# Performance work log

Measured on AMD Instinct MI355X. Metric: run time of the kernel, lower is better.

The kernel has to match this reference:

```python
import jax, jax.numpy as jnp
import numpy as np

NHEAD = 16

def setup_inputs() -> dict:
    key = jax.random.key(0)
    ks = jax.random.split(key, 7)
    b, l, d = 4, 2048, 1024
    s = 1.0 / np.sqrt(d)
    return {
        "Q": jax.random.normal(ks[0], (b, l, d), jnp.float32),
        "K": jax.random.normal(ks[1], (b, l, d), jnp.float32),
        "V": jax.random.normal(ks[2], (b, l, d), jnp.float32),
        "WQ": jax.random.normal(ks[3], (d, d), jnp.float32) * s,
        "WK": jax.random.normal(ks[4], (d, d), jnp.float32) * s,
        "WV": jax.random.normal(ks[5], (d, d), jnp.float32) * s,
        "WO": jax.random.normal(ks[6], (d, d), jnp.float32) * s,
    }

def reference(Q, K, V, WQ, WK, WV, WO):
    # WQ/WK/WV/WO stored torch-style as [out, in]; Linear(x) = x @ W.T
    b, lq, d = Q.shape
    lk = K.shape[1]
    h = NHEAD
    dk = d // h
    # project and split heads: [b, l, h, dk]
    q = (Q @ WQ.T).reshape(b, lq, h, dk)
    k = (K @ WK.T).reshape(b, lk, h, dk)
    v = (V @ WV.T).reshape(b, lk, h, dk)
    # scaled dot-product attention (dropout = identity in eval mode)
    scale = 1.0 / jnp.sqrt(jnp.asarray(dk, Q.dtype))
    score = jnp.einsum('bqhd,bkhd->bhqk', q, k) * scale  # [b,h,lq,lk]
    attn = jax.nn.softmax(score, axis=-1)
    o = jnp.einsum('bhqk,bkhd->bqhd', attn, v).reshape(b, lq, h * dk)
    return o @ WO.T
```

## Files before the change

### kernel.cpp

```cpp
#include <hip/hip_runtime.h>
#include <stdint.h>

#define D_MODEL 1024
#define NHEADS 16
#define DKH 64
#define SEQ 2048
#define BATCH 4
#define M_TOT (BATCH * SEQ)
#define LOG2E 1.44269504088896340736f

typedef __bf16 v8bf __attribute__((ext_vector_type(8)));
typedef __bf16 v4bf __attribute__((ext_vector_type(4)));
typedef _Float16 v8h __attribute__((ext_vector_type(8)));
typedef _Float16 v4h __attribute__((ext_vector_type(4)));
typedef float v4f __attribute__((ext_vector_type(4)));
typedef float v16f __attribute__((ext_vector_type(16)));
typedef unsigned int v4u __attribute__((ext_vector_type(4)));
typedef unsigned int v2u __attribute__((ext_vector_type(2)));

typedef const __attribute__((address_space(1))) void* gas_ptr;
typedef __attribute__((address_space(3))) void* las_ptr;

static __device__ __forceinline__ void async16(const void* g, void* l) {
    __builtin_amdgcn_global_load_lds((gas_ptr)g, (las_ptr)l, 16, 0, 0);
}

static __device__ __forceinline__ v4f mfma16x32(v8bf a, v8bf b, v4f c) {
    return __builtin_amdgcn_mfma_f32_16x16x32_bf16(a, b, c, 0, 0, 0);
}
static __device__ __forceinline__ v16f mfma32x16bf(v8bf a, v8bf b, v16f c) {
    return __builtin_amdgcn_mfma_f32_32x32x16_bf16(a, b, c, 0, 0, 0);
}
static __device__ __forceinline__ v16f mfma32x16h(v8h a, v8h b, v16f c) {
    return __builtin_amdgcn_mfma_f32_32x32x16_f16(a, b, c, 0, 0, 0);
}
static __device__ __forceinline__ unsigned pkh(float a, float b) {
    return __builtin_bit_cast(unsigned, __builtin_amdgcn_cvt_pkrtz(a, b));
}
static __device__ __forceinline__ void plswap(unsigned& x, unsigned& y) {
    v2u r = __builtin_amdgcn_permlane32_swap(x, y, false, false);
    x = r[0];
    y = r[1];
}
static __device__ __forceinline__ float fexp2(float x) {
#if __has_builtin(__builtin_amdgcn_exp2f)
    return __builtin_amdgcn_exp2f(x);
#else
    float r;
    asm("v_exp_f32 %0, %1" : "=v"(r) : "v"(x));
    return r;
#endif
}

__global__ __launch_bounds__(256) void cvt_x(const float* __restrict__ src,
                                             __bf16* __restrict__ dst) {
    int i = blockIdx.x * 256 + threadIdx.x;
    const float4* s = (const float4*)src;
    float4 a = s[2 * i], b = s[2 * i + 1];
    v8bf o;
    o[0] = (__bf16)a.x; o[1] = (__bf16)a.y; o[2] = (__bf16)a.z; o[3] = (__bf16)a.w;
    o[4] = (__bf16)b.x; o[5] = (__bf16)b.y; o[6] = (__bf16)b.z; o[7] = (__bf16)b.w;
    *(v8bf*)(dst + (size_t)i * 8) = o;
}

__global__ __launch_bounds__(256) void cvt_w(const float* __restrict__ w0,
                                             const float* __restrict__ w1,
                                             const float* __restrict__ w2,
                                             const float* __restrict__ w3,
                                             __bf16* __restrict__ dst) {
    int gid = blockIdx.x * 256 + threadIdx.x;
    int tsel = gid >> 17;
    int off = gid & 131071;
    const float* s = (tsel == 0) ? w0 : (tsel == 1) ? w1 : (tsel == 2) ? w2 : w3;
    const float4* sp = (const float4*)s + 2 * (size_t)off;
    float4 a = sp[0], b = sp[1];
    v8bf o;
    o[0] = (__bf16)a.x; o[1] = (__bf16)a.y; o[2] = (__bf16)a.z; o[3] = (__bf16)a.w;
    o[4] = (__bf16)b.x; o[5] = (__bf16)b.y; o[6] = (__bf16)b.z; o[7] = (__bf16)b.w;
    *(v8bf*)(dst + ((size_t)tsel << 20) + (size_t)off * 8) = o;
}

__global__ __launch_bounds__(256) void cvt_all(const float* __restrict__ Q,
                                               const float* __restrict__ K,
                                               const float* __restrict__ V,
                                               const float* __restrict__ w0,
                                               const float* __restrict__ w1,
                                               const float* __restrict__ w2,
                                               const float* __restrict__ w3,
                                               __bf16* __restrict__ xq,
                                               __bf16* __restrict__ xk,
                                               __bf16* __restrict__ xv,
                                               __bf16* __restrict__ wb) {
    const int blk = blockIdx.x;
    const float* src;
    __bf16* dst;
    size_t off8;
    if (blk < 2048) {
        int gid = blk * 256 + threadIdx.x;
        int tsel = gid >> 17;
        src = (tsel == 0) ? w0 : (tsel == 1) ? w1 : (tsel == 2) ? w2 : w3;
        dst = wb + ((size_t)tsel << 20);
        off8 = (size_t)(gid & 131071);
    } else {
        int gb = blk - 2048;
        int t = gb >> 12;
        src = (t == 0) ? Q : (t == 1) ? K : V;
        dst = (t == 0) ? xq : (t == 1) ? xk : xv;
        off8 = (size_t)((gb & 4095) * 256 + threadIdx.x);
    }
    const float4* sp = (const float4*)src + 2 * off8;
    float4 a = sp[0], b = sp[1];
    v8bf o;
    o[0] = (__bf16)a.x; o[1] = (__bf16)a.y; o[2] = (__bf16)a.z; o[3] = (__bf16)a.w;
    o[4] = (__bf16)b.x; o[5] = (__bf16)b.y; o[6] = (__bf16)b.z; o[7] = (__bf16)b.w;
    *(v8bf*)(dst + off8 * 8) = o;
}

#define GEMM_KLOOP(Abase, Wbase)                                                   \
    auto stage = [&](int bi, int k0) {                                             \
        _Pragma("unroll") for (int p = 0; p < 2; ++p) {                            \
            int rb = (p * 4 + wave) * 16;                                          \
            async16(Abase + (size_t)(rb + wrow) * D_MODEL + k0, &As[bi][rb * 32]); \
            async16(Wbase + (size_t)(rb + wrow) * D_MODEL + k0, &Bs[bi][rb * 32]); \
        }                                                                          \
    };                                                                             \
    stage(0, 0);                                                                   \
    for (int it = 0; it < D_MODEL / 32; ++it) {                                    \
        const int cur = it & 1;                                                    \
        if (it + 1 < D_MODEL / 32) {                                               \
            stage(cur ^ 1, (it + 1) * 32);                                         \
            asm volatile("s_waitcnt vmcnt(4)" ::: "memory");                       \
        } else {                                                                   \
            asm volatile("s_waitcnt vmcnt(0)" ::: "memory");                       \
        }                                                                          \
        __builtin_amdgcn_s_barrier();                                              \
        __builtin_amdgcn_sched_barrier(0);                                         \
        v8bf af[4], bfr[4];                                                        \
        _Pragma("unroll") for (int mt = 0; mt < 4; ++mt)                           \
            af[mt] = *(const v8bf*)&As[cur][(mw + mt * 16 + r) * 32 + rdpos];      \
        _Pragma("unroll") for (int nt = 0; nt < 4; ++nt)                           \
            bfr[nt] = *(const v8bf*)&Bs[cur][(nw + nt * 16 + r) * 32 + rdpos];     \
        _Pragma("unroll") for (int mt = 0; mt < 4; ++mt)                           \
            _Pragma("unroll") for (int nt = 0; nt < 4; ++nt)                       \
                acc[mt][nt] = mfma16x32(af[mt], bfr[nt], acc[mt][nt]);             \
        asm volatile("s_waitcnt lgkmcnt(0)" ::: "memory");                         \
        __builtin_amdgcn_s_barrier();                                              \
    }

template <int LAYOUT>
__global__ __launch_bounds__(256) void gemm_nt(const __bf16* __restrict__ A,
                                               const __bf16* __restrict__ W,
                                               void* __restrict__ Cv, float scale) {
    const int t = threadIdx.x, lane = t & 63, wave = t >> 6;
    const int r = lane & 15, qd = lane >> 4;
    const int m0 = blockIdx.x * 128, n0 = blockIdx.y * 128;
    const int mw = (wave & 1) * 64, nw = (wave >> 1) * 64;

    __shared__ __align__(16) __bf16 As[2][128 * 32];
    __shared__ __align__(16) __bf16 Bs[2][128 * 32];

    const int wc = (lane & 3) ^ ((lane >> 3) & 3);
    const int wrow = lane >> 2;
    const int rdpos = (qd ^ ((r >> 1) & 3)) * 8;

    const __bf16* Ab = A + (size_t)m0 * D_MODEL + wc * 8;
    const __bf16* Wb = W + (size_t)n0 * D_MODEL + wc * 8;

    v4f acc[4][4] = {};
    GEMM_KLOOP(Ab, Wb)

#pragma unroll
    for (int mt = 0; mt < 4; ++mt)
#pragma unroll
        for (int nt = 0; nt < 4; ++nt) {
            int row = m0 + mw + mt * 16 + qd * 4;
            int col = n0 + nw + nt * 16 + r;
            if (LAYOUT == 0) {
                float* C = (float*)Cv;
#pragma unroll
                for (int i = 0; i < 4; ++i)
                    C[(size_t)(row + i) * D_MODEL + col] = acc[mt][nt][i];
            } else {
                int bb = row >> 11, l = row & (SEQ - 1);
                int h = col >> 6, d = col & (DKH - 1);
                if (LAYOUT == 2) {
                    _Float16* vt = (_Float16*)Cv;
                    v4h o;
#pragma unroll
                    for (int i = 0; i < 4; ++i) o[i] = (_Float16)acc[mt][nt][i];
                    *(v4h*)&vt[((size_t)((bb * NHEADS + h) * DKH + d)) * SEQ + l] = o;
                } else {
                    __bf16* dst = (__bf16*)Cv;
#pragma unroll
                    for (int i = 0; i < 4; ++i)
                        dst[(((size_t)(bb * NHEADS + h) * SEQ) + l + i) * DKH + d] =
                            (__bf16)(acc[mt][nt][i] * scale);
                }
            }
        }
}

__global__ __launch_bounds__(256) void gemm_qkv(const __bf16* __restrict__ xq,
                                                const __bf16* __restrict__ xk,
                                                const __bf16* __restrict__ xv,
                                                const __bf16* __restrict__ wb,
                                                __bf16* __restrict__ qh,
                                                __bf16* __restrict__ kh,
                                                _Float16* __restrict__ vtb, float qs) {
    const int z = blockIdx.z;
    const __bf16* A = (z == 0) ? xq : (z == 1) ? xk : xv;
    const __bf16* W = wb + (size_t)z * D_MODEL * D_MODEL;

    const int t = threadIdx.x, lane = t & 63, wave = t >> 6;
    const int r = lane & 15, qd = lane >> 4;
    const int m0 = blockIdx.x * 128, n0 = blockIdx.y * 128;
    const int mw = (wave & 1) * 64, nw = (wave >> 1) * 64;

    __shared__ __align__(16) __bf16 As[2][128 * 32];
    __shared__ __align__(16) __bf16 Bs[2][128 * 32];

    const int wc = (lane & 3) ^ ((lane >> 3) & 3);
    const int wrow = lane >> 2;
    const int rdpos = (qd ^ ((r >> 1) & 3)) * 8;

    const __bf16* Ab = A + (size_t)m0 * D_MODEL + wc * 8;
    const __bf16* Wb = W + (size_t)n0 * D_MODEL + wc * 8;

    v4f acc[4][4] = {};
    GEMM_KLOOP(Ab, Wb)

    const float scale = (z == 0) ? qs : 1.0f;
#pragma unroll
    for (int mt = 0; mt < 4; ++mt)
#pragma unroll
        for (int nt = 0; nt < 4; ++nt) {
            int row = m0 + mw + mt * 16 + qd * 4;
            int col = n0 + nw + nt * 16 + r;
            int bb = row >> 11, l = row & (SEQ - 1);
            int h = col >> 6, d = col & (DKH - 1);
            if (z == 2) {
                v4h o;
#pragma unroll
                for (int i = 0; i < 4; ++i) o[i] = (_Float16)acc[mt][nt][i];
                *(v4h*)&vtb[((size_t)((bb * NHEADS + h) * DKH + d)) * SEQ + l] = o;
            } else {
                __bf16* dst = (z == 0) ? qh : kh;
#pragma unroll
                for (int i = 0; i < 4; ++i)
                    dst[(((size_t)(bb * NHEADS + h) * SEQ) + l + i) * DKH + d] =
                        (__bf16)(acc[mt][nt][i] * scale);
            }
        }
}

__global__ __launch_bounds__(256, 2) void attn_kernel(const __bf16* __restrict__ qh,
                                                      const __bf16* __restrict__ kh,
                                                      const _Float16* __restrict__ vt,
                                                      __bf16* __restrict__ oh) {
    const int lane = threadIdx.x & 63, wave = threadIdx.x >> 6;
    const int l31 = lane & 31, hi = lane >> 5, l7 = lane & 7;
    const int id = blockIdx.x;
    const int bh = (id & 7) * 8 + ((id >> 3) & 7);
    const int q0 = (id >> 6) * 128 + wave * 32;

    __shared__ __align__(16) __bf16 Kb[2][64 * 64];
    __shared__ __align__(16) _Float16 Vb[2][64 * 64];

    const __bf16* kbh = kh + (size_t)bh * SEQ * DKH;
    const _Float16* vbh = vt + (size_t)bh * DKH * SEQ;

    v8bf qf[4];
#pragma unroll
    for (int c = 0; c < 4; ++c)
        qf[c] = *(const v8bf*)&qh[((size_t)bh * SEQ + q0 + l31) * DKH + c * 16 + hi * 8];

    v16f oacc[2] = {};
    float ps = 0.f;
    const v16f dz = {};

    const int srow = lane >> 3;
    const int sc = (lane & 7) ^ srow;

#pragma unroll
    for (int p = 0; p < 2; ++p) {
        int rb = wave * 16 + p * 8;
        async16(kbh + (size_t)(rb + srow) * DKH + sc * 8, &Kb[0][rb * 64]);
        async16(vbh + (size_t)(rb + srow) * SEQ + sc * 8, &Vb[0][rb * 64]);
    }

    for (int tt = 0; tt < SEQ / 64; ++tt) {
        const int buf = tt & 1;
        __syncthreads();
        if (tt + 1 < SEQ / 64) {
            const int t0 = (tt + 1) * 64;
#pragma unroll
            for (int p = 0; p < 2; ++p) {
                int rb = wave * 16 + p * 8;
                async16(kbh + (size_t)(t0 + rb + srow) * DKH + sc * 8, &Kb[buf ^ 1][rb * 64]);
                async16(vbh + (size_t)(rb + srow) * SEQ + t0 + sc * 8, &Vb[buf ^ 1][rb * 64]);
            }
        }
        const __bf16* Kc = Kb[buf];
        const _Float16* Vc = Vb[buf];
#pragma unroll
        for (int kb = 0; kb < 2; ++kb) {
            v8bf ka[4];
#pragma unroll
            for (int c = 0; c < 4; ++c)
                ka[c] = *(const v8bf*)&Kc[(kb * 32 + l31) * 64 + (((c * 2 + hi) ^ l7) << 3)];
            v16f d = mfma32x16bf(ka[0], qf[0], dz);
#pragma unroll
            for (int c = 1; c < 4; ++c) d = mfma32x16bf(ka[c], qf[c], d);
            float e[16];
#pragma unroll
            for (int i = 0; i < 16; ++i) e[i] = fexp2(d[i]);
            ps += (((e[0] + e[1]) + (e[2] + e[3])) + ((e[4] + e[5]) + (e[6] + e[7]))) +
                  (((e[8] + e[9]) + (e[10] + e[11])) + ((e[12] + e[13]) + (e[14] + e[15])));
            v8h pb[2];
#pragma unroll
            for (int kc = 0; kc < 2; ++kc) {
                unsigned a0 = pkh(e[kc * 8 + 0], e[kc * 8 + 1]);
                unsigned a1 = pkh(e[kc * 8 + 2], e[kc * 8 + 3]);
                unsigned b0 = pkh(e[kc * 8 + 4], e[kc * 8 + 5]);
                unsigned b1 = pkh(e[kc * 8 + 6], e[kc * 8 + 7]);
                plswap(a0, b0);
                plswap(a1, b1);
                v4u w = {a0, a1, b0, b1};
                pb[kc] = __builtin_bit_cast(v8h, w);
            }
#pragma unroll
            for (int dg = 0; dg < 2; ++dg)
#pragma unroll
                for (int kc = 0; kc < 2; ++kc) {
                    v8h va = *(const v8h*)&Vc[(dg * 32 + l31) * 64 +
                                              (((kb * 4 + kc * 2 + hi) ^ l7) << 3)];
                    oacc[dg] = mfma32x16h(va, pb[kc], oacc[dg]);
                }
        }
    }

    const int b = bh >> 4, h = bh & (NHEADS - 1);
    float tot = ps + __shfl_xor(ps, 32, 64);
    float inv = 1.0f / tot;
    int lq = q0 + l31;
    __bf16* op = oh + (((size_t)(b * SEQ + lq)) * NHEADS + h) * DKH;
#pragma unroll
    for (int dg = 0; dg < 2; ++dg)
#pragma unroll
        for (int g = 0; g < 4; ++g) {
            v4bf ov;
#pragma unroll
            for (int i = 0; i < 4; ++i) ov[i] = (__bf16)(oacc[dg][g * 4 + i] * inv);
            *(v4bf*)(op + dg * 32 + g * 8 + hi * 4) = ov;
        }
}

extern "C" void kernel_launch(void* const* d_in, const int* in_sizes, int n_in,
                              void* d_out, int out_size, void* d_ws, size_t ws_size,
                              hipStream_t stream) {
    const float* Q = (const float*)d_in[0];
    const float* K = (const float*)d_in[1];
    const float* V = (const float*)d_in[2];
    const float* WQ = (const float*)d_in[3];
    const float* WK = (const float*)d_in[4];
    const float* WV = (const float*)d_in[5];
    const float* WO = (const float*)d_in[6];
    float* out = (float*)d_out;

    const size_t elems = (size_t)M_TOT * D_MODEL;
    const size_t welems = (size_t)D_MODEL * D_MODEL;
    const size_t fused_need = 8 * welems + 6 * 2 * elems;

    dim3 gg(M_TOT / 128, D_MODEL / 128);

    if (ws_size >= fused_need) {
        __bf16* wb = (__bf16*)d_ws;
        __bf16* xq = wb + 4 * welems;
        __bf16* xk = xq + elems;
        __bf16* xv = xk + elems;
        __bf16* qh = xv + elems;
        __bf16* kh = qh + elems;
        _Float16* vtb = (_Float16*)(kh + elems);
        __bf16* oh = xq;

        cvt_all<<<14336, 256, 0, stream>>>(Q, K, V, WQ, WK, WV, WO, xq, xk, xv, wb);
        dim3 gz(M_TOT / 128, D_MODEL / 128, 3);
        gemm_qkv<<<gz, 256, 0, stream>>>(xq, xk, xv, wb, qh, kh, vtb, 0.125f * LOG2E);
        attn_kernel<<<1024, 256, 0, stream>>>(qh, kh, vtb, oh);
        gemm_nt<0><<<gg, 256, 0, stream>>>(oh, wb + 3 * welems, out, 1.0f);
    } else {
        __bf16* wb = (__bf16*)d_ws;
        __bf16* xb = wb + 4 * welems;
        __bf16* qh = xb + elems;
        __bf16* kh = qh + elems;
        _Float16* vtb = (_Float16*)(kh + elems);
        __bf16* oh = (__bf16*)(vtb + elems);

        cvt_w<<<2048, 256, 0, stream>>>(WQ, WK, WV, WO, wb);
        cvt_x<<<4096, 256, 0, stream>>>(Q, xb);
        gemm_nt<1><<<gg, 256, 0, stream>>>(xb, wb, qh, 0.125f * LOG2E);
        cvt_x<<<4096, 256, 0, stream>>>(K, xb);
        gemm_nt<1><<<gg, 256, 0, stream>>>(xb, wb + welems, kh, 1.0f);
        cvt_x<<<4096, 256, 0, stream>>>(V, xb);
        gemm_nt<2><<<gg, 256, 0, stream>>>(xb, wb + 2 * welems, vtb, 1.0f);
        attn_kernel<<<1024, 256, 0, stream>>>(qh, kh, vtb, oh);
        gemm_nt<0><<<gg, 256, 0, stream>>>(oh, wb + 3 * welems, out, 1.0f);
    }
}
```

Baseline: 344.1 us.

## Triple-buffer GEMM LDS stages and process two query tiles per attention wave

The GEMM k-loop moves from a double to a triple LDS buffer, which removes the trailing wait and barrier at the end of each iteration. The attention kernel now gives each wave 64 query rows (two 32-row tiles), so each K/V fragment loaded from LDS feeds twice as many MFMAs, and the grid is halved to 512 blocks. The cost is more registers per wave for two accumulators, lower grid parallelism, and a larger LDS footprint in the GEMMs. With three stages a buffer can be overwritten by a fast wave while a slower wave may still be reading it, since only one barrier per iteration remains.

```diff
diff --git a/kernel.cpp b/kernel.cpp
--- a/kernel.cpp
+++ b/kernel.cpp
@@ -126,9 +126,9 @@
     };                                                                             \
     stage(0, 0);                                                                   \
     for (int it = 0; it < D_MODEL / 32; ++it) {                                    \
-        const int cur = it & 1;                                                    \
+        const int cur = it % 3;                                                    \
         if (it + 1 < D_MODEL / 32) {                                               \
-            stage(cur ^ 1, (it + 1) * 32);                                         \
+            stage((it + 1) % 3, (it + 1) * 32);                                    \
             asm volatile("s_waitcnt vmcnt(4)" ::: "memory");                       \
         } else {                                                                   \
             asm volatile("s_waitcnt vmcnt(0)" ::: "memory");                       \
@@ -143,8 +143,6 @@
         _Pragma("unroll") for (int mt = 0; mt < 4; ++mt)                           \
             _Pragma("unroll") for (int nt = 0; nt < 4; ++nt)                       \
                 acc[mt][nt] = mfma16x32(af[mt], bfr[nt], acc[mt][nt]);             \
-        asm volatile("s_waitcnt lgkmcnt(0)" ::: "memory");                         \
-        __builtin_amdgcn_s_barrier();                                              \
     }
 
 template <int LAYOUT>
@@ -156,8 +154,8 @@
     const int m0 = blockIdx.x * 128, n0 = blockIdx.y * 128;
     const int mw = (wave & 1) * 64, nw = (wave >> 1) * 64;
 
-    __shared__ __align__(16) __bf16 As[2][128 * 32];
-    __shared__ __align__(16) __bf16 Bs[2][128 * 32];
+    __shared__ __align__(16) __bf16 As[3][128 * 32];
+    __shared__ __align__(16) __bf16 Bs[3][128 * 32];
 
     const int wc = (lane & 3) ^ ((lane >> 3) & 3);
     const int wrow = lane >> 2;
@@ -216,8 +214,8 @@
     const int m0 = blockIdx.x * 128, n0 = blockIdx.y * 128;
     const int mw = (wave & 1) * 64, nw = (wave >> 1) * 64;
 
-    __shared__ __align__(16) __bf16 As[2][128 * 32];
-    __shared__ __align__(16) __bf16 Bs[2][128 * 32];
+    __shared__ __align__(16) __bf16 As[3][128 * 32];
+    __shared__ __align__(16) __bf16 Bs[3][128 * 32];
 
     const int wc = (lane & 3) ^ ((lane >> 3) & 3);
     const int wrow = lane >> 2;
@@ -261,7 +259,7 @@
     const int l31 = lane & 31, hi = lane >> 5, l7 = lane & 7;
     const int id = blockIdx.x;
     const int bh = (id & 7) * 8 + ((id >> 3) & 7);
-    const int q0 = (id >> 6) * 128 + wave * 32;
+    const int q0 = (id >> 6) * 256 + wave * 64;
 
     __shared__ __align__(16) __bf16 Kb[2][64 * 64];
     __shared__ __align__(16) _Float16 Vb[2][64 * 64];
@@ -269,13 +267,16 @@
     const __bf16* kbh = kh + (size_t)bh * SEQ * DKH;
     const _Float16* vbh = vt + (size_t)bh * DKH * SEQ;
 
-    v8bf qf[4];
-#pragma unroll
-    for (int c = 0; c < 4; ++c)
-        qf[c] = *(const v8bf*)&qh[((size_t)bh * SEQ + q0 + l31) * DKH + c * 16 + hi * 8];
-
-    v16f oacc[2] = {};
-    float ps = 0.f;
+    v8bf qf[2][4];
+#pragma unroll
+    for (int qa = 0; qa < 2; ++qa)
+#pragma unroll
+        for (int c = 0; c < 4; ++c)
+            qf[qa][c] = *(const v8bf*)&qh[((size_t)bh * SEQ + q0 + qa * 32 + l31) * DKH +
+                                          c * 16 + hi * 8];
+
+    v16f oacc[2][2] = {};
+    float ps[2] = {0.f, 0.f};
     const v16f dz = {};
 
     const int srow = lane >> 3;
@@ -308,25 +309,28 @@
 #pragma unroll
             for (int c = 0; c < 4; ++c)
                 ka[c] = *(const v8bf*)&Kc[(kb * 32 + l31) * 64 + (((c * 2 + hi) ^ l7) << 3)];
-            v16f d = mfma32x16bf(ka[0], qf[0], dz);
-#pragma unroll
-            for (int c = 1; c < 4; ++c) d = mfma32x16bf(ka[c], qf[c], d);
-            float e[16];
-#pragma unroll
-            for (int i = 0; i < 16; ++i) e[i] = fexp2(d[i]);
-            ps += (((e[0] + e[1]) + (e[2] + e[3])) + ((e[4] + e[5]) + (e[6] + e[7]))) +
-                  (((e[8] + e[9]) + (e[10] + e[11])) + ((e[12] + e[13]) + (e[14] + e[15])));
-            v8h pb[2];
-#pragma unroll
-            for (int kc = 0; kc < 2; ++kc) {
-                unsigned a0 = pkh(e[kc * 8 + 0], e[kc * 8 + 1]);
-                unsigned a1 = pkh(e[kc * 8 + 2], e[kc * 8 + 3]);
-                unsigned b0 = pkh(e[kc * 8 + 4], e[kc * 8 + 5]);
-                unsigned b1 = pkh(e[kc * 8 + 6], e[kc * 8 + 7]);
-                plswap(a0, b0);
-                plswap(a1, b1);
-                v4u w = {a0, a1, b0, b1};
-                pb[kc] = __builtin_bit_cast(v8h, w);
+            v8h pb[2][2];
+#pragma unroll
+            for (int qa = 0; qa < 2; ++qa) {
+                v16f d = mfma32x16bf(ka[0], qf[qa][0], dz);
+#pragma unroll
+                for (int c = 1; c < 4; ++c) d = mfma32x16bf(ka[c], qf[qa][c], d);
+                float e[16];
+#pragma unroll
+                for (int i = 0; i < 16; ++i) e[i] = fexp2(d[i]);
+                ps[qa] += (((e[0] + e[1]) + (e[2] + e[3])) + ((e[4] + e[5]) + (e[6] + e[7]))) +
+                          (((e[8] + e[9]) + (e[10] + e[11])) + ((e[12] + e[13]) + (e[14] + e[15])));
+#pragma unroll
+                for (int kc = 0; kc < 2; ++kc) {
+                    unsigned a0 = pkh(e[kc * 8 + 0], e[kc * 8 + 1]);
+                    unsigned a1 = pkh(e[kc * 8 + 2], e[kc * 8 + 3]);
+                    unsigned b0 = pkh(e[kc * 8 + 4], e[kc * 8 + 5]);
+                    unsigned b1 = pkh(e[kc * 8 + 6], e[kc * 8 + 7]);
+                    plswap(a0, b0);
+                    plswap(a1, b1);
+                    v4u w = {a0, a1, b0, b1};
+                    pb[qa][kc] = __builtin_bit_cast(v8h, w);
+                }
             }
 #pragma unroll
             for (int dg = 0; dg < 2; ++dg)
@@ -334,25 +338,30 @@
                 for (int kc = 0; kc < 2; ++kc) {
                     v8h va = *(const v8h*)&Vc[(dg * 32 + l31) * 64 +
                                               (((kb * 4 + kc * 2 + hi) ^ l7) << 3)];
-                    oacc[dg] = mfma32x16h(va, pb[kc], oacc[dg]);
+#pragma unroll
+                    for (int qa = 0; qa < 2; ++qa)
+                        oacc[qa][dg] = mfma32x16h(va, pb[qa][kc], oacc[qa][dg]);
                 }
         }
     }
 
     const int b = bh >> 4, h = bh & (NHEADS - 1);
-    float tot = ps + __shfl_xor(ps, 32, 64);
-    float inv = 1.0f / tot;
-    int lq = q0 + l31;
-    __bf16* op = oh + (((size_t)(b * SEQ + lq)) * NHEADS + h) * DKH;
-#pragma unroll
-    for (int dg = 0; dg < 2; ++dg)
-#pragma unroll
-        for (int g = 0; g < 4; ++g) {
-            v4bf ov;
-#pragma unroll
-            for (int i = 0; i < 4; ++i) ov[i] = (__bf16)(oacc[dg][g * 4 + i] * inv);
-            *(v4bf*)(op + dg * 32 + g * 8 + hi * 4) = ov;
-        }
+#pragma unroll
+    for (int qa = 0; qa < 2; ++qa) {
+        float tot = ps[qa] + __shfl_xor(ps[qa], 32, 64);
+        float inv = 1.0f / tot;
+        int lq = q0 + qa * 32 + l31;
+        __bf16* op = oh + (((size_t)(b * SEQ + lq)) * NHEADS + h) * DKH;
+#pragma unroll
+        for (int dg = 0; dg < 2; ++dg)
+#pragma unroll
+            for (int g = 0; g < 4; ++g) {
+                v4bf ov;
+#pragma unroll
+                for (int i = 0; i < 4; ++i) ov[i] = (__bf16)(oacc[qa][dg][g * 4 + i] * inv);
+                *(v4bf*)(op + dg * 32 + g * 8 + hi * 4) = ov;
+            }
+    }
 }
 
 extern "C" void kernel_launch(void* const* d_in, const int* in_sizes, int n_in,
@@ -386,7 +395,7 @@
         cvt_all<<<14336, 256, 0, stream>>>(Q, K, V, WQ, WK, WV, WO, xq, xk, xv, wb);
         dim3 gz(M_TOT / 128, D_MODEL / 128, 3);
         gemm_qkv<<<gz, 256, 0, stream>>>(xq, xk, xv, wb, qh, kh, vtb, 0.125f * LOG2E);
-        attn_kernel<<<1024, 256, 0, stream>>>(qh, kh, vtb, oh);
+        attn_kernel<<<512, 256, 0, stream>>>(qh, kh, vtb, oh);
         gemm_nt<0><<<gg, 256, 0, stream>>>(oh, wb + 3 * welems, out, 1.0f);
     } else {
         __bf16* wb = (__bf16*)d_ws;
@@ -403,7 +412,7 @@
         gemm_nt<1><<<gg, 256, 0, stream>>>(xb, wb + welems, kh, 1.0f);
         cvt_x<<<4096, 256, 0, stream>>>(V, xb);
         gemm_nt<2><<<gg, 256, 0, stream>>>(xb, wb + 2 * welems, vtb, 1.0f);
-        attn_kernel<<<1024, 256, 0, stream>>>(qh, kh, vtb, oh);
+        attn_kernel<<<512, 256, 0, stream>>>(qh, kh, vtb, oh);
         gemm_nt<0><<<gg, 256, 0, stream>>>(oh, wb + 3 * welems, out, 1.0f);
     }
 }
```

Measured after the change: 317.9 us. -7.6%, faster.
